# Kernel tuning notes

Hardware: AMD Instinct MI355X
Metric: run time of the kernel (lower is better)

The kernel has to match this reference:

```python
import math
import jax, jax.numpy as jnp
import numpy as np

D_MODEL = 1024
N_HEADS = 16
D_HEAD = D_MODEL // N_HEADS


def setup_inputs() -> dict:
    key = jax.random.key(0)
    kx, kqkv, ko = jax.random.split(key, 3)
    B, T = 4, 2048
    x = jax.random.normal(kx, (B, T, D_MODEL), dtype=jnp.float32)
    # Linear(d_model, 3*d_model, bias=False): weight stored as [out, in]
    s = 1.0 / math.sqrt(D_MODEL)
    W_qkv = jax.random.uniform(kqkv, (3 * D_MODEL, D_MODEL), dtype=jnp.float32, minval=-s, maxval=s)
    W_o = jax.random.uniform(ko, (D_MODEL, D_MODEL), dtype=jnp.float32, minval=-s, maxval=s)
    return {"x": x, "W_qkv": W_qkv, "W_o": W_o}


def reference(x, W_qkv, W_o):
    B, T, C = x.shape
    H, Dh = N_HEADS, D_HEAD
    qkv = jnp.einsum('btc,oc->bto', x, W_qkv)            # [B,T,3C]
    qkv = qkv.reshape(B, T, 3, H, Dh)
    q = jnp.transpose(qkv[:, :, 0], (0, 2, 1, 3))        # [B,H,T,Dh]
    k = jnp.transpose(qkv[:, :, 1], (0, 2, 1, 3))
    v = jnp.transpose(qkv[:, :, 2], (0, 2, 1, 3))
    scale = 1.0 / math.sqrt(Dh)
    attn = jnp.einsum('bhqd,bhkd->bhqk', q, k) * scale   # [B,H,T,T]
    causal = jnp.tril(jnp.ones((T, T), dtype=bool))
    attn = jnp.where(causal, attn, -jnp.inf)
    attn = jax.nn.softmax(attn, axis=-1)
    out = jnp.einsum('bhqk,bhkd->bhqd', attn, v)         # [B,H,T,Dh]
    out = jnp.transpose(out, (0, 2, 1, 3)).reshape(B, T, C)
    return jnp.einsum('btc,oc->bto', out, W_o)
```

## Files before the change

### kernel.cpp

```cpp
#include <hip/hip_runtime.h>
#include <hip/hip_bf16.h>
#include <cstdint>

#define TT      2048
#define NBATCH  4
#define BTROWS  8192
#define CDIM    1024
#define NQKV    3072
#define QSCALE  0.18033688011112042f

using bf16x8 = __attribute__((ext_vector_type(8))) short;
using f32x4  = __attribute__((ext_vector_type(4))) float;
using f32x16 = __attribute__((ext_vector_type(16))) float;

#define GLOAD_LDS16(g, l)                                                     \
  __builtin_amdgcn_global_load_lds(                                           \
      (const __attribute__((address_space(1))) unsigned int*)(g),             \
      (__attribute__((address_space(3))) unsigned int*)(l), 16, 0, 0)

__device__ inline short f2bf(float f) {
  unsigned u = __builtin_bit_cast(unsigned, f);
  u += 0x7FFF + ((u >> 16) & 1);
  return (short)(u >> 16);
}

__global__ __launch_bounds__(256) void conv_bf16(const float* __restrict__ in,
                                                 short* __restrict__ out, int n) {
  int i = (blockIdx.x * 256 + threadIdx.x) * 4;
  if (i + 3 < n) {
    float4 v = *(const float4*)(in + i);
    short4 o;
    o.x = f2bf(v.x); o.y = f2bf(v.y); o.z = f2bf(v.z); o.w = f2bf(v.w);
    *(short4*)(out + i) = o;
  }
}

__global__ __launch_bounds__(256) void gemm_qkv(const short* __restrict__ A,
                                                const short* __restrict__ Bw,
                                                short* __restrict__ Qb,
                                                short* __restrict__ Kb,
                                                short* __restrict__ Vb) {
  const int K = CDIM;
  __shared__ __attribute__((aligned(16))) short As[128 * 32];
  __shared__ __attribute__((aligned(16))) short Bs[128 * 32];
  int tid = threadIdx.x;
  int bm = blockIdx.x, bn = blockIdx.y;
  int lane = tid & 63, wid = tid >> 6;
  int wr = wid >> 1, wc = wid & 1;
  int la = lane & 15, lg = lane >> 4;

  const short* Ab = A + (size_t)bm * 128 * K;
  const short* Bb = Bw + (size_t)bn * 128 * K;

  f32x4 acc[4][4];
#pragma unroll
  for (int m = 0; m < 4; m++)
#pragma unroll
    for (int n = 0; n < 4; n++) acc[m][n] = (f32x4){0.f, 0.f, 0.f, 0.f};

  int c0 = tid, c1 = tid + 256;
  for (int k0 = 0; k0 < K; k0 += 32) {
    GLOAD_LDS16(Ab + (c0 >> 2) * K + k0 + (c0 & 3) * 8, &As[c0 * 8]);
    GLOAD_LDS16(Ab + (c1 >> 2) * K + k0 + (c1 & 3) * 8, &As[c1 * 8]);
    GLOAD_LDS16(Bb + (c0 >> 2) * K + k0 + (c0 & 3) * 8, &Bs[c0 * 8]);
    GLOAD_LDS16(Bb + (c1 >> 2) * K + k0 + (c1 & 3) * 8, &Bs[c1 * 8]);
    __syncthreads();
    bf16x8 af[4], bfr[4];
#pragma unroll
    for (int m = 0; m < 4; m++)
      af[m] = *(const bf16x8*)&As[(wr * 64 + m * 16 + la) * 32 + lg * 8];
#pragma unroll
    for (int n = 0; n < 4; n++)
      bfr[n] = *(const bf16x8*)&Bs[(wc * 64 + n * 16 + la) * 32 + lg * 8];
#pragma unroll
    for (int m = 0; m < 4; m++)
#pragma unroll
      for (int n = 0; n < 4; n++)
        acc[m][n] = __builtin_amdgcn_mfma_f32_16x16x32_bf16(af[m], bfr[n],
                                                            acc[m][n], 0, 0, 0);
    __syncthreads();
  }

#pragma unroll
  for (int m = 0; m < 4; m++) {
    int rbase = bm * 128 + wr * 64 + m * 16 + lg * 4;
    int b = rbase >> 11;
    int tb = rbase & 2047;
#pragma unroll
    for (int n = 0; n < 4; n++) {
      int col = bn * 128 + wc * 64 + n * 16 + la;
      int which = col >> 10;
      int h = (col >> 6) & 15;
      int d = col & 63;
      if (which == 2) {
        short4 o4;
        o4.x = f2bf(acc[m][n][0]); o4.y = f2bf(acc[m][n][1]);
        o4.z = f2bf(acc[m][n][2]); o4.w = f2bf(acc[m][n][3]);
        *(short4*)&Vb[((size_t)(b * 16 + h) * 64 + d) * TT + tb] = o4;
      } else {
        short* dst = (which == 0) ? Qb : Kb;
        float sc = (which == 0) ? QSCALE : 1.0f;
        size_t base = ((size_t)(b * 16 + h) * TT) * 64 + d;
#pragma unroll
        for (int r = 0; r < 4; r++)
          dst[base + (size_t)(tb + r) * 64] = f2bf(acc[m][n][r] * sc);
      }
    }
  }
}

__global__ __launch_bounds__(256, 4) void attn_fwd2(const short* __restrict__ Qb,
                                                    const short* __restrict__ Kb,
                                                    const short* __restrict__ Vtg,
                                                    short* __restrict__ Ob) {
  __shared__ __attribute__((aligned(16))) short lds[10240];
  short* Ks = lds;
  short* Vs = lds + 4096;

  int tid = threadIdx.x, lane = tid & 63, w = tid >> 6;
  int l31 = lane & 31, hi = lane >> 5, l7 = lane & 7;
  int gid = blockIdx.x;
  int qt = 15 - (gid & 15);
  int bh = gid >> 4;
  int q0 = qt * 128;
  int qw = q0 + w * 32;
  int qg = qw + l31;

  const short* Qh = Qb + (size_t)bh * TT * 64;
  const short* Kh = Kb + (size_t)bh * TT * 64;
  const short* Vh = Vtg + (size_t)bh * 64 * TT;

  bf16x8 q[4];
#pragma unroll
  for (int c = 0; c < 4; c++)
    q[c] = *(const bf16x8*)(Qh + (size_t)qg * 64 + c * 16 + hi * 8);

  f32x16 o0, o1;
#pragma unroll
  for (int r = 0; r < 16; r++) { o0[r] = 0.f; o1[r] = 0.f; }
  float m = -1e30f, lsum = 0.f;

  int nt = 2 * qt + 2;
  int c0 = tid, c1 = tid + 256;
  int r0 = c0 >> 3, cc0 = c0 & 7;
  int r1 = c1 >> 3, cc1 = c1 & 7;

  bf16x8 kr0, kr1, vr0, vr1;
  kr0 = *(const bf16x8*)(Kh + (size_t)r0 * 64 + cc0 * 8);
  kr1 = *(const bf16x8*)(Kh + (size_t)r1 * 64 + cc1 * 8);
  vr0 = *(const bf16x8*)(Vh + (size_t)r0 * TT + cc0 * 8);
  vr1 = *(const bf16x8*)(Vh + (size_t)r1 * TT + cc1 * 8);

  for (int it = 0; it < nt; it++) {
    int kv0 = it * 64;
    __syncthreads();
    *(bf16x8*)&Ks[r0 * 64 + ((cc0 ^ (r0 & 7)) * 8)] = kr0;
    *(bf16x8*)&Ks[r1 * 64 + ((cc1 ^ (r1 & 7)) * 8)] = kr1;
    *(bf16x8*)&Vs[r0 * 64 + ((cc0 ^ (r0 & 7)) * 8)] = vr0;
    *(bf16x8*)&Vs[r1 * 64 + ((cc1 ^ (r1 & 7)) * 8)] = vr1;
    __syncthreads();
    if (it + 1 < nt) {
      int kn = kv0 + 64;
      kr0 = *(const bf16x8*)(Kh + (size_t)(kn + r0) * 64 + cc0 * 8);
      kr1 = *(const bf16x8*)(Kh + (size_t)(kn + r1) * 64 + cc1 * 8);
      vr0 = *(const bf16x8*)(Vh + (size_t)r0 * TT + kn + cc0 * 8);
      vr1 = *(const bf16x8*)(Vh + (size_t)r1 * TT + kn + cc1 * 8);
    }
    if (kv0 <= qw + 31) {
      f32x16 st0, st1;
#pragma unroll
      for (int r = 0; r < 16; r++) { st0[r] = 0.f; st1[r] = 0.f; }
#pragma unroll
      for (int c = 0; c < 4; c++) {
        int cc = c * 2 + hi;
        bf16x8 kf0 = *(const bf16x8*)&Ks[l31 * 64 + ((cc ^ l7) * 8)];
        bf16x8 kf1 = *(const bf16x8*)&Ks[(32 + l31) * 64 + ((cc ^ l7) * 8)];
        st0 = __builtin_amdgcn_mfma_f32_32x32x16_bf16(kf0, q[c], st0, 0, 0, 0);
        st1 = __builtin_amdgcn_mfma_f32_32x32x16_bf16(kf1, q[c], st1, 0, 0, 0);
      }
      if (kv0 + 63 > qw) {
#pragma unroll
        for (int r = 0; r < 16; r++) {
          int kloc = (r & 3) + 8 * (r >> 2) + 4 * hi;
          if (kv0 + kloc > qg)      st0[r] = -1e30f;
          if (kv0 + 32 + kloc > qg) st1[r] = -1e30f;
        }
      }
      float pm = -1e30f;
#pragma unroll
      for (int r = 0; r < 16; r++) {
        pm = fmaxf(pm, st0[r]); pm = fmaxf(pm, st1[r]);
      }
      pm = fmaxf(pm, __shfl_xor(pm, 32));
      if (!__all(pm <= m + 8.f)) {
        float mn = fmaxf(m, pm);
        float fac = exp2f(m - mn);
        lsum *= fac;
#pragma unroll
        for (int r = 0; r < 16; r++) { o0[r] *= fac; o1[r] *= fac; }
        m = mn;
      }
      float rs = 0.f;
#pragma unroll
      for (int r = 0; r < 16; r++) {
        st0[r] = exp2f(st0[r] - m); rs += st0[r];
        st1[r] = exp2f(st1[r] - m); rs += st1[r];
      }
      rs += __shfl_xor(rs, 32);
      lsum += rs;
#pragma unroll
      for (int kb = 0; kb < 2; kb++) {
#pragma unroll
        for (int c2 = 0; c2 < 2; c2++) {
          float p0 = kb ? st1[8 * c2 + 0] : st0[8 * c2 + 0];
          float p1 = kb ? st1[8 * c2 + 1] : st0[8 * c2 + 1];
          float p2 = kb ? st1[8 * c2 + 2] : st0[8 * c2 + 2];
          float p3 = kb ? st1[8 * c2 + 3] : st0[8 * c2 + 3];
          float p4 = kb ? st1[8 * c2 + 4] : st0[8 * c2 + 4];
          float p5 = kb ? st1[8 * c2 + 5] : st0[8 * c2 + 5];
          float p6 = kb ? st1[8 * c2 + 6] : st0[8 * c2 + 6];
          float p7 = kb ? st1[8 * c2 + 7] : st0[8 * c2 + 7];
          unsigned u0, u1, u2, u3;
          asm("v_cvt_pk_bf16_f32 %0, %1, %2" : "=v"(u0) : "v"(p0), "v"(p1));
          asm("v_cvt_pk_bf16_f32 %0, %1, %2" : "=v"(u1) : "v"(p2), "v"(p3));
          asm("v_cvt_pk_bf16_f32 %0, %1, %2" : "=v"(u2) : "v"(p4), "v"(p5));
          asm("v_cvt_pk_bf16_f32 %0, %1, %2" : "=v"(u3) : "v"(p6), "v"(p7));
          asm volatile("v_permlane32_swap_b32 %0, %1" : "+v"(u0), "+v"(u2));
          asm volatile("v_permlane32_swap_b32 %0, %1" : "+v"(u1), "+v"(u3));
          union { unsigned u[4]; bf16x8 v; } pa;
          pa.u[0] = u0; pa.u[1] = u1; pa.u[2] = u2; pa.u[3] = u3;
          int ccv = kb * 4 + c2 * 2 + hi;
          bf16x8 vf0 = *(const bf16x8*)&Vs[l31 * 64 + ((ccv ^ l7) * 8)];
          bf16x8 vf1 = *(const bf16x8*)&Vs[(32 + l31) * 64 + ((ccv ^ l7) * 8)];
          o0 = __builtin_amdgcn_mfma_f32_32x32x16_bf16(vf0, pa.v, o0, 0, 0, 0);
          o1 = __builtin_amdgcn_mfma_f32_32x32x16_bf16(vf1, pa.v, o1, 0, 0, 0);
        }
      }
    }
  }

  __syncthreads();
  short* Os = lds + w * (32 * 80);
  float inv = 1.f / lsum;
#pragma unroll
  for (int k = 0; k < 4; k++) {
    float a0 = o0[4 * k + 0] * inv, a1 = o0[4 * k + 1] * inv;
    float a2 = o0[4 * k + 2] * inv, a3 = o0[4 * k + 3] * inv;
    float b0 = o1[4 * k + 0] * inv, b1 = o1[4 * k + 1] * inv;
    float b2 = o1[4 * k + 2] * inv, b3 = o1[4 * k + 3] * inv;
    unsigned w0, w1, w2, w3;
    asm("v_cvt_pk_bf16_f32 %0, %1, %2" : "=v"(w0) : "v"(a0), "v"(a1));
    asm("v_cvt_pk_bf16_f32 %0, %1, %2" : "=v"(w1) : "v"(a2), "v"(a3));
    asm("v_cvt_pk_bf16_f32 %0, %1, %2" : "=v"(w2) : "v"(b0), "v"(b1));
    asm("v_cvt_pk_bf16_f32 %0, %1, %2" : "=v"(w3) : "v"(b2), "v"(b3));
    int d = 8 * k + 4 * hi;
    uint2 pa; pa.x = w0; pa.y = w1;
    uint2 pb; pb.x = w2; pb.y = w3;
    *(uint2*)&Os[l31 * 80 + d] = pa;
    *(uint2*)&Os[l31 * 80 + 32 + d] = pb;
  }
  __syncthreads();
  int b = bh >> 4, h = bh & 15;
#pragma unroll
  for (int pass = 0; pass < 4; pass++) {
    int qr = pass * 8 + (lane >> 3);
    int cc = lane & 7;
    bf16x8 v = *(const bf16x8*)&Os[qr * 80 + cc * 8];
    *(bf16x8*)&Ob[((size_t)(b * TT + q0 + w * 32 + qr)) * CDIM + h * 64 + cc * 8] = v;
  }
}

__global__ __launch_bounds__(256) void gemm_out(const short* __restrict__ A,
                                                const short* __restrict__ Bw,
                                                float* __restrict__ C) {
  const int K = CDIM;
  __shared__ __attribute__((aligned(16))) short As[128 * 32];
  __shared__ __attribute__((aligned(16))) short Bs[128 * 32];
  int tid = threadIdx.x;
  int bm = blockIdx.x, bn = blockIdx.y;
  int lane = tid & 63, wid = tid >> 6;
  int wr = wid >> 1, wc = wid & 1;
  int la = lane & 15, lg = lane >> 4;

  const short* Ab = A + (size_t)bm * 128 * K;
  const short* Bb = Bw + (size_t)bn * 128 * K;

  f32x4 acc[4][4];
#pragma unroll
  for (int m = 0; m < 4; m++)
#pragma unroll
    for (int n = 0; n < 4; n++) acc[m][n] = (f32x4){0.f, 0.f, 0.f, 0.f};

  int c0 = tid, c1 = tid + 256;
  for (int k0 = 0; k0 < K; k0 += 32) {
    GLOAD_LDS16(Ab + (c0 >> 2) * K + k0 + (c0 & 3) * 8, &As[c0 * 8]);
    GLOAD_LDS16(Ab + (c1 >> 2) * K + k0 + (c1 & 3) * 8, &As[c1 * 8]);
    GLOAD_LDS16(Bb + (c0 >> 2) * K + k0 + (c0 & 3) * 8, &Bs[c0 * 8]);
    GLOAD_LDS16(Bb + (c1 >> 2) * K + k0 + (c1 & 3) * 8, &Bs[c1 * 8]);
    __syncthreads();
    bf16x8 af[4], bfr[4];
#pragma unroll
    for (int m = 0; m < 4; m++)
      af[m] = *(const bf16x8*)&As[(wr * 64 + m * 16 + la) * 32 + lg * 8];
#pragma unroll
    for (int n = 0; n < 4; n++)
      bfr[n] = *(const bf16x8*)&Bs[(wc * 64 + n * 16 + la) * 32 + lg * 8];
#pragma unroll
    for (int m = 0; m < 4; m++)
#pragma unroll
      for (int n = 0; n < 4; n++)
        acc[m][n] = __builtin_amdgcn_mfma_f32_16x16x32_bf16(af[m], bfr[n],
                                                            acc[m][n], 0, 0, 0);
    __syncthreads();
  }

#pragma unroll
  for (int m = 0; m < 4; m++) {
    int rbase = bm * 128 + wr * 64 + m * 16 + lg * 4;
#pragma unroll
    for (int n = 0; n < 4; n++) {
      int col = bn * 128 + wc * 64 + n * 16 + la;
#pragma unroll
      for (int r = 0; r < 4; r++)
        C[(size_t)(rbase + r) * CDIM + col] = acc[m][n][r];
    }
  }
}

extern "C" void kernel_launch(void* const* d_in, const int* in_sizes, int n_in,
                              void* d_out, int out_size, void* d_ws, size_t ws_size,
                              hipStream_t stream) {
  const float* x    = (const float*)d_in[0];
  const float* wqkv = (const float*)d_in[1];
  const float* wo   = (const float*)d_in[2];
  float* out = (float*)d_out;

  char* ws = (char*)d_ws;
  short* xb  = (short*)(ws);
  short* wqb = (short*)(ws + (size_t)(16 << 20));
  short* wob = (short*)(ws + (size_t)(22 << 20));
  short* Qb  = (short*)(ws + (size_t)(24 << 20));
  short* Kb  = (short*)(ws + (size_t)(40 << 20));
  short* Vb  = (short*)(ws + (size_t)(56 << 20));
  short* Ob  = (short*)(ws + (size_t)(72 << 20));

  conv_bf16<<<8192, 256, 0, stream>>>(x, xb, BTROWS * CDIM);
  conv_bf16<<<3072, 256, 0, stream>>>(wqkv, wqb, NQKV * CDIM);
  conv_bf16<<<1024, 256, 0, stream>>>(wo, wob, CDIM * CDIM);

  gemm_qkv<<<dim3(BTROWS / 128, NQKV / 128), 256, 0, stream>>>(xb, wqb, Qb, Kb, Vb);
  attn_fwd2<<<NBATCH * 16 * (TT / 128), 256, 0, stream>>>(Qb, Kb, Vb, Ob);
  gemm_out<<<dim3(BTROWS / 128, CDIM / 128), 256, 0, stream>>>(Ob, wob, out);
}
```

Before: 317.7 us.

## Swizzle GEMM block order, tree-reduce softmax max/sum, relax attention launch bounds

Both GEMMs now remap blockIdx.x with a bit-swizzle so that consecutively scheduled blocks spread across M, aiming for better L2/XCD locality. In attention, the per-row max and sum reductions become pairwise trees instead of serial chains, shortening dependency latency. The attention kernel drops the min-4-blocks occupancy hint, which gives the compiler more registers but may reduce occupancy.

```diff
diff --git a/kernel.cpp b/kernel.cpp
--- a/kernel.cpp
+++ b/kernel.cpp
@@ -44,7 +44,9 @@
   __shared__ __attribute__((aligned(16))) short As[128 * 32];
   __shared__ __attribute__((aligned(16))) short Bs[128 * 32];
   int tid = threadIdx.x;
-  int bm = blockIdx.x, bn = blockIdx.y;
+  int bid = blockIdx.x;
+  int bm = ((bid & 7) << 3) | (bid >> 3);
+  int bn = blockIdx.y;
   int lane = tid & 63, wid = tid >> 6;
   int wr = wid >> 1, wc = wid & 1;
   int la = lane & 15, lg = lane >> 4;
@@ -109,10 +111,10 @@
   }
 }
 
-__global__ __launch_bounds__(256, 4) void attn_fwd2(const short* __restrict__ Qb,
-                                                    const short* __restrict__ Kb,
-                                                    const short* __restrict__ Vtg,
-                                                    short* __restrict__ Ob) {
+__global__ __launch_bounds__(256) void attn_fwd2(const short* __restrict__ Qb,
+                                                 const short* __restrict__ Kb,
+                                                 const short* __restrict__ Vtg,
+                                                 short* __restrict__ Ob) {
   __shared__ __attribute__((aligned(16))) short lds[10240];
   short* Ks = lds;
   short* Vs = lds + 4096;
@@ -186,11 +188,15 @@
           if (kv0 + 32 + kloc > qg) st1[r] = -1e30f;
         }
       }
-      float pm = -1e30f;
-#pragma unroll
-      for (int r = 0; r < 16; r++) {
-        pm = fmaxf(pm, st0[r]); pm = fmaxf(pm, st1[r]);
-      }
+      float tm[16];
+#pragma unroll
+      for (int r = 0; r < 16; r++) tm[r] = fmaxf(st0[r], st1[r]);
+#pragma unroll
+      for (int s = 8; s >= 1; s >>= 1)
+#pragma unroll
+        for (int r = 0; r < 16; r++)
+          if (r < s) tm[r] = fmaxf(tm[r], tm[r + s]);
+      float pm = tm[0];
       pm = fmaxf(pm, __shfl_xor(pm, 32));
       if (!__all(pm <= m + 8.f)) {
         float mn = fmaxf(m, pm);
@@ -200,12 +206,19 @@
         for (int r = 0; r < 16; r++) { o0[r] *= fac; o1[r] *= fac; }
         m = mn;
       }
-      float rs = 0.f;
+      float ts[16];
 #pragma unroll
       for (int r = 0; r < 16; r++) {
-        st0[r] = exp2f(st0[r] - m); rs += st0[r];
-        st1[r] = exp2f(st1[r] - m); rs += st1[r];
-      }
+        st0[r] = exp2f(st0[r] - m);
+        st1[r] = exp2f(st1[r] - m);
+        ts[r] = st0[r] + st1[r];
+      }
+#pragma unroll
+      for (int s = 8; s >= 1; s >>= 1)
+#pragma unroll
+        for (int r = 0; r < 16; r++)
+          if (r < s) ts[r] += ts[r + s];
+      float rs = ts[0];
       rs += __shfl_xor(rs, 32);
       lsum += rs;
 #pragma unroll
@@ -277,7 +290,9 @@
   __shared__ __attribute__((aligned(16))) short As[128 * 32];
   __shared__ __attribute__((aligned(16))) short Bs[128 * 32];
   int tid = threadIdx.x;
-  int bm = blockIdx.x, bn = blockIdx.y;
+  int bid = blockIdx.x;
+  int bm = ((bid & 7) << 3) | (bid >> 3);
+  int bn = blockIdx.y;
   int lane = tid & 63, wid = tid >> 6;
   int wr = wid >> 1, wc = wid & 1;
   int la = lane & 15, lg = lane >> 4;
```

Result: slower. 332.4 us (+4.6%).
